# Performance work log

Measured on AMD Instinct MI355X. Metric: run time of the kernel, lower is better.

The kernel has to match this reference:

```python
import jax, jax.numpy as jnp
import numpy as np
from jax import lax

# Pipeline constants (forward defaults / __init__ defaults of OVDDetector)
B, N, C = 16, 4096, 64
TARGET = 602.0          # target_size
IOU_THR = 0.2           # iou_thr
CONF_THRES = 0.001      # conf_thres (final detection confidence)
BOX_CONF_THR = 0.01     # box_conf_threshold (RPN objectness filter)
MIN_BOX = 5.0           # min_box_size
MAX_WH = 4096.0         # per-class box offset for class-aware NMS (yolo-style)
NEG_INF = -1e9


def setup_inputs() -> dict:
    key = jax.random.key(0)
    k1, k2, k3, k4 = jax.random.split(key, 4)
    # Build valid xyxy proposals inside the image: centers + positive sizes.
    cxcy = jax.random.uniform(k1, (B, N, 2)) * TARGET
    wh = jax.random.uniform(k2, (B, N, 2)) * 200.0 + 1.0
    proposals = jnp.concatenate([cxcy - wh / 2, cxcy + wh / 2], axis=-1)  # [B,N,4]
    proposals_scores = jax.random.uniform(k3, (B, N))                     # [B,N] objectness
    # Classifier outputs are normalized per-class similarities (normalize=True).
    preds = jax.nn.softmax(jax.random.normal(k4, (B, N, C)), axis=-1)      # [B,N,C]
    return {"proposals": proposals, "preds": preds, "proposals_scores": proposals_scores}


def _iou_matrix(b):
    # b: [N,4] xyxy -> [N,N] pairwise IoU
    area = jnp.maximum(b[:, 2] - b[:, 0], 0.0) * jnp.maximum(b[:, 3] - b[:, 1], 0.0)
    lt = jnp.maximum(b[:, None, :2], b[None, :, :2])
    rb = jnp.minimum(b[:, None, 2:], b[None, :, 2:])
    whi = jnp.maximum(rb - lt, 0.0)
    inter = whi[..., 0] * whi[..., 1]
    union = area[:, None] + area[None, :] - inter
    return inter / (union + 1e-7)


def _process_one(boxes, cls_preds, obj_scores):
    # boxes [N,4], cls_preds [N,C], obj_scores [N]
    # --- filter_boxes: objectness threshold, clip to image, drop tiny boxes ---
    boxes = jnp.clip(boxes, 0.0, TARGET)
    w = boxes[:, 2] - boxes[:, 0]
    h = boxes[:, 3] - boxes[:, 1]
    valid = (obj_scores > BOX_CONF_THR) & (w >= MIN_BOX) & (h >= MIN_BOX)
    # --- yolo-style NMS prep: class conf = cls_score * obj_score ---
    cls_conf = cls_preds * obj_scores[:, None]           # [N,C]
    conf = jnp.max(cls_conf, axis=-1)                    # [N]
    cls = jnp.argmax(cls_conf, axis=-1)                  # [N] int
    valid = valid & (conf > CONF_THRES)
    # --- sort descending by confidence (invalid pushed to the end) ---
    order = jnp.argsort(-jnp.where(valid, conf, NEG_INF))
    boxes_s = boxes[order]
    conf_s = conf[order]
    cls_s = cls[order]
    valid_s = valid[order]
    # --- class-aware greedy NMS via per-class coordinate offset ---
    off_boxes = boxes_s + (cls_s.astype(boxes_s.dtype) * MAX_WH)[:, None]
    iou = _iou_matrix(off_boxes)                         # [N,N]
    idx = jnp.arange(N)

    def body(keep, i):
        suppress = (iou[i] > IOU_THR) & keep[i] & (idx > i)
        return keep & ~suppress, None

    keep, _ = lax.scan(body, valid_s, idx)
    out = jnp.concatenate(
        [boxes_s, conf_s[:, None], cls_s.astype(boxes_s.dtype)[:, None]], axis=1
    )                                                    # [N,6] = x1,y1,x2,y2,conf,cls
    out = jnp.where(keep[:, None], out, 0.0)
    return out, keep


def reference(proposals, preds, proposals_scores):
    # Returns padded detections [B,N,6] and validity mask [B,N]
    out, keep = jax.vmap(_process_one)(proposals, preds, proposals_scores)
    return out, keep
```

## Files before the change

### kernel.cpp

```cpp
#include <hip/hip_runtime.h>
#include <stdint.h>

#define B_ 16
#define N_ 4096
#define C_ 64
#define BN_ 65536

__device__ __forceinline__ float clipf(float x, float lo, float hi) {
    return fminf(fmaxf(x, lo), hi);
}
__device__ __forceinline__ float bcastf(float v, int l) {
    return __int_as_float(__builtin_amdgcn_readlane(__float_as_int(v), l));
}
__device__ __forceinline__ unsigned long long bcast64(unsigned long long v, int l) {
    unsigned int lo = (unsigned int)__builtin_amdgcn_readlane((int)(unsigned int)v, l);
    unsigned int hi = (unsigned int)__builtin_amdgcn_readlane((int)(unsigned int)(v >> 32), l);
    return ((unsigned long long)hi << 32) | lo;
}
__device__ __forceinline__ float iou_rn(
    float ax1, float ay1, float ax2, float ay2, float aar,
    float bx1, float by1, float bx2, float by2, float bar)
{
    float ltx = fmaxf(ax1, bx1), lty = fmaxf(ay1, by1);
    float rbx = fminf(ax2, bx2), rby = fminf(ay2, by2);
    float wx  = fmaxf(__fsub_rn(rbx, ltx), 0.f);
    float wy  = fmaxf(__fsub_rn(rby, lty), 0.f);
    float inter = __fmul_rn(wx, wy);
    float uni   = __fsub_rn(__fadd_rn(aar, bar), inter);
    return inter / __fadd_rn(uni, 1e-7f);
}

__global__ __launch_bounds__(256) void score_kernel(
    const float* __restrict__ proposals,
    const float* __restrict__ preds,
    const float* __restrict__ scores,
    unsigned int* __restrict__ key32,
    float* __restrict__ conf_o,
    float* __restrict__ clsf_o,
    unsigned char* __restrict__ cv_o,
    float* __restrict__ out)
{
    const int gt  = blockIdx.x * 256 + threadIdx.x;
    if (gt < BN_ * 7) out[gt] = 0.f;
    const int wid = gt >> 4;
    const int sub = gt & 15;

    float obj = scores[wid];
    float4 p4 = *reinterpret_cast<const float4*>(preds + (size_t)wid * C_ + sub * 4);
    float v; int idx;
    {
        float v0 = p4.x * obj, v1 = p4.y * obj, v2 = p4.z * obj, v3 = p4.w * obj;
        v = v0; idx = sub * 4;
        if (v1 > v) { v = v1; idx = sub * 4 + 1; }
        if (v2 > v) { v = v2; idx = sub * 4 + 2; }
        if (v3 > v) { v = v3; idx = sub * 4 + 3; }
    }
    #pragma unroll
    for (int o = 8; o > 0; o >>= 1) {
        float vv = __shfl_xor(v, o, 64);
        int   ii = __shfl_xor(idx, o, 64);
        if (vv > v || (vv == v && ii < idx)) { v = vv; idx = ii; }
    }

    if (sub == 0) {
        float4 bx = *reinterpret_cast<const float4*>(proposals + (size_t)wid * 4);
        float x1 = clipf(bx.x, 0.f, 602.f);
        float y1 = clipf(bx.y, 0.f, 602.f);
        float x2 = clipf(bx.z, 0.f, 602.f);
        float y2 = clipf(bx.w, 0.f, 602.f);
        bool valid = (obj > 0.01f) && ((x2 - x1) >= 5.f) && ((y2 - y1) >= 5.f)
                     && (v > 0.001f);
        float keyf = valid ? v : -1e9f;
        unsigned int u = __float_as_uint(keyf);
        u ^= (u >> 31) ? 0xFFFFFFFFu : 0x80000000u;
        key32[wid] = ~u;
        conf_o[wid] = v;
        clsf_o[wid] = (float)idx;
        cv_o[wid]   = valid ? (unsigned char)idx : (unsigned char)255;
    }
}

#define CE_(A, Bq)                                                              \
        {                                                                       \
            bool sw = (kr[A] > kr[Bq]) || (kr[A] == kr[Bq] && pr[A] > pr[Bq]);  \
            if (sw) {                                                           \
                unsigned int tk = kr[A]; kr[A] = kr[Bq]; kr[Bq] = tk;           \
                unsigned short tp = pr[A]; pr[A] = pr[Bq]; pr[Bq] = tp;         \
            }                                                                   \
        }

__global__ __launch_bounds__(256) void sortA_kernel(
    const unsigned int* __restrict__ key32,
    unsigned int* __restrict__ runkey,
    unsigned short* __restrict__ runpay)
{
    __shared__ unsigned int  k0[1024], k1[1024];
    __shared__ unsigned short p0[1024], p1[1024];
    const int r = blockIdx.x;
    const int t = threadIdx.x;
    const int g0 = r * 1024;

    {
        uint4 kk = *reinterpret_cast<const uint4*>(key32 + g0 + t * 4);
        unsigned int  kr[4] = {kk.x, kk.y, kk.z, kk.w};
        unsigned short pr[4] = {(unsigned short)((r & 3) * 1024 + t * 4),
                                (unsigned short)((r & 3) * 1024 + t * 4 + 1),
                                (unsigned short)((r & 3) * 1024 + t * 4 + 2),
                                (unsigned short)((r & 3) * 1024 + t * 4 + 3)};
        CE_(0, 1) CE_(2, 3) CE_(0, 2) CE_(1, 3) CE_(1, 2)
        #pragma unroll
        for (int s = 0; s < 4; ++s) { k0[t * 4 + s] = kr[s]; p0[t * 4 + s] = pr[s]; }
    }

    unsigned int*  ks = k0; unsigned int*  kd = k1;
    unsigned short* ps = p0; unsigned short* pd = p1;

    for (int dlog = 2; dlog <= 9; ++dlog) {
        const int R = 1 << dlog;
        __syncthreads();
        unsigned int  mk[4]; unsigned short mp[4];
        int lo[4], hi[4], sb[4], db[4]; bool teq[4];
        #pragma unroll
        for (int s = 0; s < 4; ++s) {
            int i = t + s * 256;
            mk[s] = ks[i]; mp[s] = ps[i];
            int base = i & ~(2 * R - 1);
            bool isA = (i & R) == 0;
            sb[s] = base + (isA ? R : 0);
            db[s] = base + (i & (R - 1));
            teq[s] = !isA;
            lo[s] = -1; hi[s] = R;
        }
        for (int it = 0; it < dlog + 1; ++it) {
            #pragma unroll
            for (int s = 0; s < 4; ++s) {
                if (hi[s] - lo[s] > 1) {
                    int mid = (lo[s] + hi[s]) >> 1;
                    unsigned int sk = ks[sb[s] + mid];
                    bool less = (sk < mk[s]) || (sk == mk[s] && teq[s]);
                    if (less) lo[s] = mid; else hi[s] = mid;
                }
            }
        }
        #pragma unroll
        for (int s = 0; s < 4; ++s) {
            kd[db[s] + hi[s]] = mk[s];
            pd[db[s] + hi[s]] = mp[s];
        }
        unsigned int*  tk = ks; ks = kd; kd = tk;
        unsigned short* tp = ps; ps = pd; pd = tp;
    }
    __syncthreads();
    #pragma unroll
    for (int s = 0; s < 4; ++s) {
        int i = t + s * 256;
        runkey[g0 + i] = ks[i];
        runpay[g0 + i] = ps[i];
    }
}

__global__ __launch_bounds__(256) void mergeG4_kernel(
    const unsigned int* __restrict__ runkey,
    const unsigned short* __restrict__ runpay,
    const float* __restrict__ proposals,
    const float* __restrict__ conf,
    const float* __restrict__ clsf,
    const unsigned char* __restrict__ cv,
    float* __restrict__ boxes_s,
    float* __restrict__ conf_s,
    float* __restrict__ clsf_s,
    unsigned char* __restrict__ cv_s)
{
    const int i = blockIdx.x * 256 + threadIdx.x;
    const int batch = i >> 12;
    const int run   = (i >> 10) & 3;
    const int p     = i & 1023;
    const unsigned int mk = runkey[i];
    const unsigned short mp = runpay[i];
    const unsigned int* kb = runkey + (batch << 12);

    int lo[3], hi[3], sb[3]; bool teq[3];
    {
        int s = 0;
        #pragma unroll
        for (int j = 0; j < 4; ++j) {
            if (j == run) continue;
            sb[s] = j << 10;
            teq[s] = (j < run);
            lo[s] = -1; hi[s] = 1024;
            ++s;
        }
    }
    for (int it = 0; it < 11; ++it) {
        #pragma unroll
        for (int s = 0; s < 3; ++s) {
            if (hi[s] - lo[s] > 1) {
                int mid = (lo[s] + hi[s]) >> 1;
                unsigned int sk = kb[sb[s] + mid];
                bool less = (sk < mk) || (sk == mk && teq[s]);
                if (less) lo[s] = mid; else hi[s] = mid;
            }
        }
    }
    int dst = (batch << 12) + p + hi[0] + hi[1] + hi[2];
    int src = (batch << 12) + (int)mp;

    float4 bx = *reinterpret_cast<const float4*>(proposals + (size_t)src * 4);
    float x1 = clipf(bx.x, 0.f, 602.f);
    float y1 = clipf(bx.y, 0.f, 602.f);
    float x2 = clipf(bx.z, 0.f, 602.f);
    float y2 = clipf(bx.w, 0.f, 602.f);
    *reinterpret_cast<float4*>(boxes_s + (size_t)dst * 4) =
        make_float4(x1, y1, x2, y2);
    conf_s[dst] = conf[src];
    clsf_s[dst] = clsf[src];
    cv_s[dst]   = cv[src];
}

__device__ __forceinline__ void emit_row(
    const float* __restrict__ boxes_s, const float* __restrict__ conf_s,
    const float* __restrict__ clsf_s, float* __restrict__ out, int row)
{
    float4 bb = *reinterpret_cast<const float4*>(boxes_s + (size_t)row * 4);
    size_t o = (size_t)row * 6;
    out[o + 0] = bb.x; out[o + 1] = bb.y;
    out[o + 2] = bb.z; out[o + 3] = bb.w;
    out[o + 4] = conf_s[row];
    out[o + 5] = clsf_s[row];
    out[(size_t)BN_ * 6 + row] = 1.f;
}

__global__ __launch_bounds__(64) void nms_kernel(
    const float* __restrict__ boxes_s,
    const float* __restrict__ conf_s,
    const float* __restrict__ clsf_s,
    const unsigned char* __restrict__ cv_s,
    float* __restrict__ out)
{
    __shared__ unsigned short flist[N_];
    __shared__ unsigned char alive8[N_];
    const int bc = blockIdx.x;
    const int b = bc >> 6, c = bc & 63;
    const int lane = threadIdx.x;
    const float offc = (float)c * 4096.0f;
    const unsigned char* cv = cv_s + (size_t)b * N_;

    int base = 0;
    #pragma unroll 16
    for (int it = 0; it < N_ / 64; ++it) {
        bool pred = cv[it * 64 + lane] == (unsigned char)c;
        unsigned long long m = __ballot(pred);
        if (pred)
            flist[base + __popcll(m & ((1ull << lane) - 1ull))] =
                (unsigned short)(it * 64 + lane);
        base += __popcll(m);
    }
    const int L = base;
    if (L <= 1) {
        if (lane < L)
            emit_row(boxes_s, conf_s, clsf_s, out, b * N_ + flist[lane]);
        return;
    }

    if (L <= 64) {
        bool in = lane < L;
        unsigned short myp = in ? flist[lane] : (unsigned short)0;
        float x1 = offc, y1 = offc, x2 = offc, y2 = offc, ar = 0.f;
        if (in) {
            float4 bb = *reinterpret_cast<const float4*>(
                boxes_s + ((size_t)b * N_ + myp) * 4);
            x1 = __fadd_rn(bb.x, offc); y1 = __fadd_rn(bb.y, offc);
            x2 = __fadd_rn(bb.z, offc); y2 = __fadd_rn(bb.w, offc);
            ar = __fmul_rn(fmaxf(__fsub_rn(x2, x1), 0.f),
                           fmaxf(__fsub_rn(y2, y1), 0.f));
        }
        unsigned long long row = 0;
        for (int j = 1; j < L; ++j) {
            float jx1 = bcastf(x1, j), jy1 = bcastf(y1, j);
            float jx2 = bcastf(x2, j), jy2 = bcastf(y2, j);
            float jar = bcastf(ar, j);
            float iou = iou_rn(jx1, jy1, jx2, jy2, jar, x1, y1, x2, y2, ar);
            if (in && j > lane && iou > 0.2f) row |= 1ull << j;
        }
        unsigned long long alive = (L >= 64) ? ~0ull : ((1ull << L) - 1ull);
        unsigned int rlo = (unsigned int)row, rhi = (unsigned int)(row >> 32);
        for (int k = 0; k < L - 1; ++k) {
            if ((alive >> k) & 1ull) {
                unsigned int lo = (unsigned int)__builtin_amdgcn_readlane((int)rlo, k);
                unsigned int hi = (unsigned int)__builtin_amdgcn_readlane((int)rhi, k);
                alive &= ~(((unsigned long long)hi << 32) | (unsigned long long)lo);
            }
        }
        if (in && ((alive >> lane) & 1ull))
            emit_row(boxes_s, conf_s, clsf_s, out, b * N_ + myp);
    } else if (L <= 128) {
        bool in1 = (64 + lane) < L;
        unsigned short myp0 = flist[lane];
        unsigned short myp1 = in1 ? flist[64 + lane] : (unsigned short)0;
        float ax1, ay1, ax2, ay2, aar;
        {
            float4 bb = *reinterpret_cast<const float4*>(
                boxes_s + ((size_t)b * N_ + myp0) * 4);
            ax1 = __fadd_rn(bb.x, offc); ay1 = __fadd_rn(bb.y, offc);
            ax2 = __fadd_rn(bb.z, offc); ay2 = __fadd_rn(bb.w, offc);
            aar = __fmul_rn(fmaxf(__fsub_rn(ax2, ax1), 0.f),
                            fmaxf(__fsub_rn(ay2, ay1), 0.f));
        }
        float bx1 = offc, by1 = offc, bx2 = offc, by2 = offc, bar = 0.f;
        if (in1) {
            float4 bb = *reinterpret_cast<const float4*>(
                boxes_s + ((size_t)b * N_ + myp1) * 4);
            bx1 = __fadd_rn(bb.x, offc); by1 = __fadd_rn(bb.y, offc);
            bx2 = __fadd_rn(bb.z, offc); by2 = __fadd_rn(bb.w, offc);
            bar = __fmul_rn(fmaxf(__fsub_rn(bx2, bx1), 0.f),
                            fmaxf(__fsub_rn(by2, by1), 0.f));
        }
        unsigned long long r0lo = 0, r0hi = 0, r1hi = 0;
        for (int j = 1; j < 64; ++j) {
            float jx1 = bcastf(ax1, j), jy1 = bcastf(ay1, j);
            float jx2 = bcastf(ax2, j), jy2 = bcastf(ay2, j);
            float jar = bcastf(aar, j);
            float i0 = iou_rn(jx1, jy1, jx2, jy2, jar, ax1, ay1, ax2, ay2, aar);
            if (j > lane && i0 > 0.2f) r0lo |= 1ull << j;
        }
        const int Lh = L - 64;
        for (int jm = 0; jm < Lh; ++jm) {
            float jx1 = bcastf(bx1, jm), jy1 = bcastf(by1, jm);
            float jx2 = bcastf(bx2, jm), jy2 = bcastf(by2, jm);
            float jar = bcastf(bar, jm);
            float i0 = iou_rn(jx1, jy1, jx2, jy2, jar, ax1, ay1, ax2, ay2, aar);
            if (i0 > 0.2f) r0hi |= 1ull << jm;
            float i1 = iou_rn(jx1, jy1, jx2, jy2, jar, bx1, by1, bx2, by2, bar);
            if (in1 && jm > lane && i1 > 0.2f) r1hi |= 1ull << jm;
        }
        unsigned long long alo = ~0ull;
        unsigned long long ahi = (Lh >= 64) ? ~0ull : ((1ull << Lh) - 1ull);
        for (int k = 0; k < 64; ++k) {
            if ((alo >> k) & 1ull) {
                alo &= ~bcast64(r0lo, k);
                ahi &= ~bcast64(r0hi, k);
            }
        }
        for (int k = 0; k < Lh - 1; ++k) {
            if ((ahi >> k) & 1ull) ahi &= ~bcast64(r1hi, k);
        }
        if ((alo >> lane) & 1ull)
            emit_row(boxes_s, conf_s, clsf_s, out, b * N_ + myp0);
        if (in1 && ((ahi >> lane) & 1ull))
            emit_row(boxes_s, conf_s, clsf_s, out, b * N_ + myp1);
    } else {
        for (int j = lane; j < L; j += 64) alive8[j] = 1;
        for (int k = 0; k < L - 1; ++k) {
            if (!alive8[k]) continue;
            float4 kb = *reinterpret_cast<const float4*>(
                boxes_s + ((size_t)b * N_ + flist[k]) * 4);
            float kx1 = __fadd_rn(kb.x, offc), ky1 = __fadd_rn(kb.y, offc);
            float kx2 = __fadd_rn(kb.z, offc), ky2 = __fadd_rn(kb.w, offc);
            float kar = __fmul_rn(fmaxf(__fsub_rn(kx2, kx1), 0.f),
                                  fmaxf(__fsub_rn(ky2, ky1), 0.f));
            for (int j = k + 1 + lane; j < L; j += 64) {
                if (!alive8[j]) continue;
                float4 bb = *reinterpret_cast<const float4*>(
                    boxes_s + ((size_t)b * N_ + flist[j]) * 4);
                float a1 = __fadd_rn(bb.x, offc), b1 = __fadd_rn(bb.y, offc);
                float a2 = __fadd_rn(bb.z, offc), b2 = __fadd_rn(bb.w, offc);
                float arj = __fmul_rn(fmaxf(__fsub_rn(a2, a1), 0.f),
                                      fmaxf(__fsub_rn(b2, b1), 0.f));
                float iou = iou_rn(kx1, ky1, kx2, ky2, kar, a1, b1, a2, b2, arj);
                if (iou > 0.2f) alive8[j] = 0;
            }
        }
        for (int j = lane; j < L; j += 64)
            if (alive8[j])
                emit_row(boxes_s, conf_s, clsf_s, out, b * N_ + flist[j]);
    }
}

extern "C" void kernel_launch(void* const* d_in, const int* in_sizes, int n_in,
                              void* d_out, int out_size, void* d_ws, size_t ws_size,
                              hipStream_t stream) {
    (void)in_sizes; (void)n_in; (void)out_size; (void)ws_size;
    const float* proposals = (const float*)d_in[0];
    const float* preds     = (const float*)d_in[1];
    const float* scores    = (const float*)d_in[2];
    float* out = (float*)d_out;

    uint8_t* w = (uint8_t*)d_ws;
    unsigned int* key32    = (unsigned int*)(w);
    float* conf            = (float*)(w + (size_t)BN_ * 4);
    float* clsf            = (float*)(w + (size_t)BN_ * 8);
    unsigned int* runkey   = (unsigned int*)(w + (size_t)BN_ * 12);
    float* boxes_s         = (float*)(w + (size_t)BN_ * 16);
    float* conf_s          = (float*)(w + (size_t)BN_ * 32);
    float* clsf_s          = (float*)(w + (size_t)BN_ * 36);
    unsigned short* runpay = (unsigned short*)(w + (size_t)BN_ * 40);
    unsigned char* cv      = w + (size_t)BN_ * 42;
    unsigned char* cv_s    = w + (size_t)BN_ * 43;

    score_kernel<<<(BN_ * 16) / 256, 256, 0, stream>>>(
        proposals, preds, scores, key32, conf, clsf, cv, out);
    sortA_kernel<<<64, 256, 0, stream>>>(key32, runkey, runpay);
    mergeG4_kernel<<<BN_ / 256, 256, 0, stream>>>(
        runkey, runpay, proposals, conf, clsf, cv,
        boxes_s, conf_s, clsf_s, cv_s);
    nms_kernel<<<B_ * C_, 64, 0, stream>>>(
        boxes_s, conf_s, clsf_s, cv_s, out);
}
```

Before: 74.15 us.

## Sort 512-element runs with 8-way rank merge and gather boxes via permutation

The block sort now produces eight 512-element runs per batch across 128 blocks of 128 threads instead of four 1024-element runs across 64 blocks. The merge kernel ranks each element against eight runs and writes only a 16-bit permutation and class-valid byte, no longer materialising sorted boxes, conf and class arrays. The NMS kernel then gathers and clips boxes from the original proposals through the permutation. This doubles sort parallelism and cuts merge-stage write traffic, at the cost of more binary searches per element and an extra indirection on every box load in NMS.

```diff
diff --git a/kernel.cpp b/kernel.cpp
--- a/kernel.cpp
+++ b/kernel.cpp
@@ -28,6 +28,13 @@
     float inter = __fmul_rn(wx, wy);
     float uni   = __fsub_rn(__fadd_rn(aar, bar), inter);
     return inter / __fadd_rn(uni, 1e-7f);
+}
+__device__ __forceinline__ float4 load_clip(const float* __restrict__ proposals,
+                                            int src)
+{
+    float4 bx = *reinterpret_cast<const float4*>(proposals + (size_t)src * 4);
+    return make_float4(clipf(bx.x, 0.f, 602.f), clipf(bx.y, 0.f, 602.f),
+                       clipf(bx.z, 0.f, 602.f), clipf(bx.w, 0.f, 602.f));
 }
 
 __global__ __launch_bounds__(256) void score_kernel(
@@ -89,24 +96,25 @@
             }                                                                   \
         }
 
-__global__ __launch_bounds__(256) void sortA_kernel(
+__global__ __launch_bounds__(128) void sortA_kernel(
     const unsigned int* __restrict__ key32,
     unsigned int* __restrict__ runkey,
     unsigned short* __restrict__ runpay)
 {
-    __shared__ unsigned int  k0[1024], k1[1024];
-    __shared__ unsigned short p0[1024], p1[1024];
-    const int r = blockIdx.x;
+    __shared__ unsigned int  k0[512], k1[512];
+    __shared__ unsigned short p0[512], p1[512];
+    const int blk = blockIdx.x;
+    const int b = blk >> 3, c = blk & 7;
     const int t = threadIdx.x;
-    const int g0 = r * 1024;
+    const int g0 = b * N_ + c * 512;
 
     {
         uint4 kk = *reinterpret_cast<const uint4*>(key32 + g0 + t * 4);
         unsigned int  kr[4] = {kk.x, kk.y, kk.z, kk.w};
-        unsigned short pr[4] = {(unsigned short)((r & 3) * 1024 + t * 4),
-                                (unsigned short)((r & 3) * 1024 + t * 4 + 1),
-                                (unsigned short)((r & 3) * 1024 + t * 4 + 2),
-                                (unsigned short)((r & 3) * 1024 + t * 4 + 3)};
+        unsigned short pr[4] = {(unsigned short)(c * 512 + t * 4),
+                                (unsigned short)(c * 512 + t * 4 + 1),
+                                (unsigned short)(c * 512 + t * 4 + 2),
+                                (unsigned short)(c * 512 + t * 4 + 3)};
         CE_(0, 1) CE_(2, 3) CE_(0, 2) CE_(1, 3) CE_(1, 2)
         #pragma unroll
         for (int s = 0; s < 4; ++s) { k0[t * 4 + s] = kr[s]; p0[t * 4 + s] = pr[s]; }
@@ -115,14 +123,14 @@
     unsigned int*  ks = k0; unsigned int*  kd = k1;
     unsigned short* ps = p0; unsigned short* pd = p1;
 
-    for (int dlog = 2; dlog <= 9; ++dlog) {
+    for (int dlog = 2; dlog <= 8; ++dlog) {
         const int R = 1 << dlog;
         __syncthreads();
         unsigned int  mk[4]; unsigned short mp[4];
         int lo[4], hi[4], sb[4], db[4]; bool teq[4];
         #pragma unroll
         for (int s = 0; s < 4; ++s) {
-            int i = t + s * 256;
+            int i = t + s * 128;
             mk[s] = ks[i]; mp[s] = ps[i];
             int base = i & ~(2 * R - 1);
             bool isA = (i & R) == 0;
@@ -153,88 +161,70 @@
     __syncthreads();
     #pragma unroll
     for (int s = 0; s < 4; ++s) {
-        int i = t + s * 256;
+        int i = t + s * 128;
         runkey[g0 + i] = ks[i];
         runpay[g0 + i] = ps[i];
     }
 }
 
-__global__ __launch_bounds__(256) void mergeG4_kernel(
+__global__ __launch_bounds__(256) void rank8_kernel(
     const unsigned int* __restrict__ runkey,
     const unsigned short* __restrict__ runpay,
+    const unsigned char* __restrict__ cv,
+    unsigned short* __restrict__ perm,
+    unsigned char* __restrict__ cv_s)
+{
+    const int i = blockIdx.x * 256 + threadIdx.x;
+    const int batch = i >> 12;
+    const int run   = (i >> 9) & 7;
+    const int p     = i & 511;
+    const unsigned int mk = runkey[i];
+    const unsigned short mp = runpay[i];
+    const unsigned int* kb = runkey + (batch << 12);
+
+    int lo[8], hi[8];
+    #pragma unroll
+    for (int j = 0; j < 8; ++j) { lo[j] = -1; hi[j] = 512; }
+    for (int it = 0; it < 10; ++it) {
+        #pragma unroll
+        for (int j = 0; j < 8; ++j) {
+            if (hi[j] - lo[j] > 1) {
+                int mid = (lo[j] + hi[j]) >> 1;
+                unsigned int sk = kb[(j << 9) + mid];
+                bool less = (sk < mk) || (sk == mk && (j < run));
+                if (less) lo[j] = mid; else hi[j] = mid;
+            }
+        }
+    }
+    int dst = (batch << 12) + p;
+    #pragma unroll
+    for (int j = 0; j < 8; ++j) dst += (j == run) ? 0 : hi[j];
+
+    perm[dst] = mp;
+    cv_s[dst] = cv[(batch << 12) + (int)mp];
+}
+
+__device__ __forceinline__ void emit_row(
+    const float* __restrict__ proposals, const float* __restrict__ conf,
+    const float* __restrict__ clsf, const unsigned short* __restrict__ perm,
+    float* __restrict__ out, int row)
+{
+    int src = (row & ~(N_ - 1)) | (int)perm[row];
+    float4 bb = load_clip(proposals, src);
+    size_t o = (size_t)row * 6;
+    out[o + 0] = bb.x; out[o + 1] = bb.y;
+    out[o + 2] = bb.z; out[o + 3] = bb.w;
+    out[o + 4] = conf[src];
+    out[o + 5] = clsf[src];
+    out[(size_t)BN_ * 6 + row] = 1.f;
+}
+
+__global__ __launch_bounds__(64) void nms_kernel(
     const float* __restrict__ proposals,
     const float* __restrict__ conf,
     const float* __restrict__ clsf,
-    const unsigned char* __restrict__ cv,
-    float* __restrict__ boxes_s,
-    float* __restrict__ conf_s,
-    float* __restrict__ clsf_s,
-    unsigned char* __restrict__ cv_s)
-{
-    const int i = blockIdx.x * 256 + threadIdx.x;
-    const int batch = i >> 12;
-    const int run   = (i >> 10) & 3;
-    const int p     = i & 1023;
-    const unsigned int mk = runkey[i];
-    const unsigned short mp = runpay[i];
-    const unsigned int* kb = runkey + (batch << 12);
-
-    int lo[3], hi[3], sb[3]; bool teq[3];
-    {
-        int s = 0;
-        #pragma unroll
-        for (int j = 0; j < 4; ++j) {
-            if (j == run) continue;
-            sb[s] = j << 10;
-            teq[s] = (j < run);
-            lo[s] = -1; hi[s] = 1024;
-            ++s;
-        }
-    }
-    for (int it = 0; it < 11; ++it) {
-        #pragma unroll
-        for (int s = 0; s < 3; ++s) {
-            if (hi[s] - lo[s] > 1) {
-                int mid = (lo[s] + hi[s]) >> 1;
-                unsigned int sk = kb[sb[s] + mid];
-                bool less = (sk < mk) || (sk == mk && teq[s]);
-                if (less) lo[s] = mid; else hi[s] = mid;
-            }
-        }
-    }
-    int dst = (batch << 12) + p + hi[0] + hi[1] + hi[2];
-    int src = (batch << 12) + (int)mp;
-
-    float4 bx = *reinterpret_cast<const float4*>(proposals + (size_t)src * 4);
-    float x1 = clipf(bx.x, 0.f, 602.f);
-    float y1 = clipf(bx.y, 0.f, 602.f);
-    float x2 = clipf(bx.z, 0.f, 602.f);
-    float y2 = clipf(bx.w, 0.f, 602.f);
-    *reinterpret_cast<float4*>(boxes_s + (size_t)dst * 4) =
-        make_float4(x1, y1, x2, y2);
-    conf_s[dst] = conf[src];
-    clsf_s[dst] = clsf[src];
-    cv_s[dst]   = cv[src];
-}
-
-__device__ __forceinline__ void emit_row(
-    const float* __restrict__ boxes_s, const float* __restrict__ conf_s,
-    const float* __restrict__ clsf_s, float* __restrict__ out, int row)
-{
-    float4 bb = *reinterpret_cast<const float4*>(boxes_s + (size_t)row * 4);
-    size_t o = (size_t)row * 6;
-    out[o + 0] = bb.x; out[o + 1] = bb.y;
-    out[o + 2] = bb.z; out[o + 3] = bb.w;
-    out[o + 4] = conf_s[row];
-    out[o + 5] = clsf_s[row];
-    out[(size_t)BN_ * 6 + row] = 1.f;
-}
-
-__global__ __launch_bounds__(64) void nms_kernel(
-    const float* __restrict__ boxes_s,
-    const float* __restrict__ conf_s,
-    const float* __restrict__ clsf_s,
     const unsigned char* __restrict__ cv_s,
+    const unsigned short* __restrict__ perm,
     float* __restrict__ out)
 {
     __shared__ unsigned short flist[N_];
@@ -244,6 +234,7 @@
     const int lane = threadIdx.x;
     const float offc = (float)c * 4096.0f;
     const unsigned char* cv = cv_s + (size_t)b * N_;
+    const unsigned short* pm = perm + (size_t)b * N_;
 
     int base = 0;
     #pragma unroll 16
@@ -258,7 +249,7 @@
     const int L = base;
     if (L <= 1) {
         if (lane < L)
-            emit_row(boxes_s, conf_s, clsf_s, out, b * N_ + flist[lane]);
+            emit_row(proposals, conf, clsf, perm, out, b * N_ + flist[lane]);
         return;
     }
 
@@ -267,8 +258,8 @@
         unsigned short myp = in ? flist[lane] : (unsigned short)0;
         float x1 = offc, y1 = offc, x2 = offc, y2 = offc, ar = 0.f;
         if (in) {
-            float4 bb = *reinterpret_cast<const float4*>(
-                boxes_s + ((size_t)b * N_ + myp) * 4);
+            int src = (b << 12) + (int)pm[myp];
+            float4 bb = load_clip(proposals, src);
             x1 = __fadd_rn(bb.x, offc); y1 = __fadd_rn(bb.y, offc);
             x2 = __fadd_rn(bb.z, offc); y2 = __fadd_rn(bb.w, offc);
             ar = __fmul_rn(fmaxf(__fsub_rn(x2, x1), 0.f),
@@ -292,15 +283,15 @@
             }
         }
         if (in && ((alive >> lane) & 1ull))
-            emit_row(boxes_s, conf_s, clsf_s, out, b * N_ + myp);
+            emit_row(proposals, conf, clsf, perm, out, b * N_ + myp);
     } else if (L <= 128) {
         bool in1 = (64 + lane) < L;
         unsigned short myp0 = flist[lane];
         unsigned short myp1 = in1 ? flist[64 + lane] : (unsigned short)0;
         float ax1, ay1, ax2, ay2, aar;
         {
-            float4 bb = *reinterpret_cast<const float4*>(
-                boxes_s + ((size_t)b * N_ + myp0) * 4);
+            int src = (b << 12) + (int)pm[myp0];
+            float4 bb = load_clip(proposals, src);
             ax1 = __fadd_rn(bb.x, offc); ay1 = __fadd_rn(bb.y, offc);
             ax2 = __fadd_rn(bb.z, offc); ay2 = __fadd_rn(bb.w, offc);
             aar = __fmul_rn(fmaxf(__fsub_rn(ax2, ax1), 0.f),
@@ -308,8 +299,8 @@
         }
         float bx1 = offc, by1 = offc, bx2 = offc, by2 = offc, bar = 0.f;
         if (in1) {
-            float4 bb = *reinterpret_cast<const float4*>(
-                boxes_s + ((size_t)b * N_ + myp1) * 4);
+            int src = (b << 12) + (int)pm[myp1];
+            float4 bb = load_clip(proposals, src);
             bx1 = __fadd_rn(bb.x, offc); by1 = __fadd_rn(bb.y, offc);
             bx2 = __fadd_rn(bb.z, offc); by2 = __fadd_rn(bb.w, offc);
             bar = __fmul_rn(fmaxf(__fsub_rn(bx2, bx1), 0.f),
@@ -345,23 +336,23 @@
             if ((ahi >> k) & 1ull) ahi &= ~bcast64(r1hi, k);
         }
         if ((alo >> lane) & 1ull)
-            emit_row(boxes_s, conf_s, clsf_s, out, b * N_ + myp0);
+            emit_row(proposals, conf, clsf, perm, out, b * N_ + myp0);
         if (in1 && ((ahi >> lane) & 1ull))
-            emit_row(boxes_s, conf_s, clsf_s, out, b * N_ + myp1);
+            emit_row(proposals, conf, clsf, perm, out, b * N_ + myp1);
     } else {
         for (int j = lane; j < L; j += 64) alive8[j] = 1;
         for (int k = 0; k < L - 1; ++k) {
             if (!alive8[k]) continue;
-            float4 kb = *reinterpret_cast<const float4*>(
-                boxes_s + ((size_t)b * N_ + flist[k]) * 4);
+            int ksrc = (b << 12) + (int)pm[flist[k]];
+            float4 kb = load_clip(proposals, ksrc);
             float kx1 = __fadd_rn(kb.x, offc), ky1 = __fadd_rn(kb.y, offc);
             float kx2 = __fadd_rn(kb.z, offc), ky2 = __fadd_rn(kb.w, offc);
             float kar = __fmul_rn(fmaxf(__fsub_rn(kx2, kx1), 0.f),
                                   fmaxf(__fsub_rn(ky2, ky1), 0.f));
             for (int j = k + 1 + lane; j < L; j += 64) {
                 if (!alive8[j]) continue;
-                float4 bb = *reinterpret_cast<const float4*>(
-                    boxes_s + ((size_t)b * N_ + flist[j]) * 4);
+                int jsrc = (b << 12) + (int)pm[flist[j]];
+                float4 bb = load_clip(proposals, jsrc);
                 float a1 = __fadd_rn(bb.x, offc), b1 = __fadd_rn(bb.y, offc);
                 float a2 = __fadd_rn(bb.z, offc), b2 = __fadd_rn(bb.w, offc);
                 float arj = __fmul_rn(fmaxf(__fsub_rn(a2, a1), 0.f),
@@ -372,7 +363,7 @@
         }
         for (int j = lane; j < L; j += 64)
             if (alive8[j])
-                emit_row(boxes_s, conf_s, clsf_s, out, b * N_ + flist[j]);
+                emit_row(proposals, conf, clsf, perm, out, b * N_ + flist[j]);
     }
 }
 
@@ -390,19 +381,16 @@
     float* conf            = (float*)(w + (size_t)BN_ * 4);
     float* clsf            = (float*)(w + (size_t)BN_ * 8);
     unsigned int* runkey   = (unsigned int*)(w + (size_t)BN_ * 12);
-    float* boxes_s         = (float*)(w + (size_t)BN_ * 16);
-    float* conf_s          = (float*)(w + (size_t)BN_ * 32);
-    float* clsf_s          = (float*)(w + (size_t)BN_ * 36);
-    unsigned short* runpay = (unsigned short*)(w + (size_t)BN_ * 40);
-    unsigned char* cv      = w + (size_t)BN_ * 42;
-    unsigned char* cv_s    = w + (size_t)BN_ * 43;
+    unsigned short* runpay = (unsigned short*)(w + (size_t)BN_ * 16);
+    unsigned short* perm   = (unsigned short*)(w + (size_t)BN_ * 18);
+    unsigned char* cv      = w + (size_t)BN_ * 20;
+    unsigned char* cv_s    = w + (size_t)BN_ * 21;
 
     score_kernel<<<(BN_ * 16) / 256, 256, 0, stream>>>(
         proposals, preds, scores, key32, conf, clsf, cv, out);
-    sortA_kernel<<<64, 256, 0, stream>>>(key32, runkey, runpay);
-    mergeG4_kernel<<<BN_ / 256, 256, 0, stream>>>(
-        runkey, runpay, proposals, conf, clsf, cv,
-        boxes_s, conf_s, clsf_s, cv_s);
+    sortA_kernel<<<128, 128, 0, stream>>>(key32, runkey, runpay);
+    rank8_kernel<<<BN_ / 256, 256, 0, stream>>>(
+        runkey, runpay, cv, perm, cv_s);
     nms_kernel<<<B_ * C_, 64, 0, stream>>>(
-        boxes_s, conf_s, clsf_s, cv_s, out);
-}
+        proposals, conf, clsf, cv_s, perm, out);
+}
```

Result: slower. 78.79 us (+6.2%).
